# Kernel optimization log

Measured on AMD Instinct MI355X. Metric: run time of the kernel, lower is better.

The kernel has to match this reference:

```python
import jax, jax.numpy as jnp
import numpy as np

E = 1024
H = 16
HD = E // H  # 64


def setup_inputs() -> dict:
    key = jax.random.key(0)
    ks = jax.random.split(key, 5)
    x = jax.random.normal(ks[0], (2, 2048, E), dtype=jnp.float32)
    s = 1.0 / np.sqrt(E)
    W_qkv = jax.random.uniform(ks[1], (E, 3 * E), jnp.float32, -s, s)
    b_qkv = jax.random.uniform(ks[2], (3 * E,), jnp.float32, -s, s)
    W_out = jax.random.uniform(ks[3], (E, E), jnp.float32, -s, s)
    b_out = jax.random.uniform(ks[4], (E,), jnp.float32, -s, s)
    return {"x": x, "W_qkv": W_qkv, "b_qkv": b_qkv, "W_out": W_out, "b_out": b_out}


def reference(x, W_qkv, b_qkv, W_out, b_out):
    B, N, _ = x.shape
    scale = HD ** (-0.5)
    qkv = x @ W_qkv + b_qkv                         # [B, N, 3E]
    qkv = qkv.reshape(B, N, H, 3 * HD)              # torch layout: per-head 3*hd chunk
    qkv = qkv.transpose(0, 2, 1, 3)                 # [B, H, N, 3*hd]
    q, k, v = jnp.split(qkv, 3, axis=-1)            # each [B, H, N, hd]
    attn = jnp.einsum('bhqd,bhkd->bhqk', q, k) * scale
    attn = jax.nn.softmax(attn, axis=-1)            # dropout is identity in eval
    out = jnp.einsum('bhqk,bhkd->bhqd', attn, v)    # [B, H, N, hd]
    out = out.transpose(0, 2, 1, 3).reshape(B, N, E)
    return out @ W_out + b_out
```

## Files before the change

### kernel.cpp

```cpp
#include <hip/hip_runtime.h>


#define SEQ 2048
#define NH  16

typedef __attribute__((ext_vector_type(8))) short short8;
typedef __attribute__((ext_vector_type(4))) short short4v;
typedef __attribute__((ext_vector_type(4))) float floatx4;
typedef __attribute__((ext_vector_type(4))) _Float16 half4;
typedef __attribute__((ext_vector_type(2))) _Float16 half2v;
typedef __attribute__((ext_vector_type(2))) __fp16 fp16x2;

#define QSCALE 0.1803368801111204f

__device__ __forceinline__ short f2bf(float f) {
    union { float f; unsigned u; } v; v.f = f;
    unsigned r = v.u + 0x7fffu + ((v.u >> 16) & 1u);
    return (short)(r >> 16);
}

__device__ __forceinline__ float fast_exp2(float x) {
#if __has_builtin(__builtin_amdgcn_exp2f)
    return __builtin_amdgcn_exp2f(x);
#else
    return exp2f(x);
#endif
}

__device__ __forceinline__ half2v cvt_pk(float a, float b) {
#if __has_builtin(__builtin_amdgcn_cvt_pkrtz)
    union { fp16x2 i; half2v o; } u;
    u.i = __builtin_amdgcn_cvt_pkrtz(a, b);
    return u.o;
#else
    half2v r; r.x = (_Float16)a; r.y = (_Float16)b; return r;
#endif
}

#define GLDS16(gp, lp)                                                          \
    __builtin_amdgcn_global_load_lds(                                           \
        (const __attribute__((address_space(1))) unsigned int*)(gp),            \
        (__attribute__((address_space(3))) unsigned int*)(lp), 16, 0, 0)

__global__ __launch_bounds__(256) void prep_kernel(
    const float* __restrict__ x,  short* __restrict__ xb,
    const float* __restrict__ wq, short* __restrict__ wqkvt,
    const float* __restrict__ wo, short* __restrict__ woutt)
{
    const int tid = threadIdx.x;
    const int b = blockIdx.x;
    if (b < 2048) {
        int i = b * 256 + tid;
        const float4* in4 = (const float4*)x + (size_t)i * 2;
        float4 a = in4[0], c = in4[1];
        short8 o = { f2bf(a.x), f2bf(a.y), f2bf(a.z), f2bf(a.w),
                     f2bf(c.x), f2bf(c.y), f2bf(c.z), f2bf(c.w) };
        *((short8*)xb + i) = o;
        return;
    }
    __shared__ float T[64][65];
    const float* in; short* out; int R, C, c0, r0;
    if (b < 2816) {
        int t = b - 2048; in = wq; out = wqkvt; R = 1024; C = 3072;
        c0 = (t % 48) * 64; r0 = (t / 48) * 64;
    } else {
        int t = b - 2816; in = wo; out = woutt; R = 1024; C = 1024;
        c0 = (t & 15) * 64; r0 = (t >> 4) * 64;
    }
#pragma unroll
    for (int it = 0; it < 4; ++it) {
        int r = it * 16 + (tid >> 4), c = (tid & 15) * 4;
        float4 v = *(const float4*)(in + (size_t)(r0 + r) * C + c0 + c);
        T[c+0][r] = v.x; T[c+1][r] = v.y; T[c+2][r] = v.z; T[c+3][r] = v.w;
    }
    __syncthreads();
#pragma unroll
    for (int it = 0; it < 4; ++it) {
        int oc = it * 16 + (tid >> 4), k = (tid & 15) * 4;
        short4v o = { f2bf(T[oc][k]), f2bf(T[oc][k+1]), f2bf(T[oc][k+2]), f2bf(T[oc][k+3]) };
        *(short4v*)(out + (size_t)(c0 + oc) * R + r0 + k) = o;
    }
}

__global__ __launch_bounds__(256) void vtrans_kernel(
    const _Float16* __restrict__ vn, _Float16* __restrict__ vt)
{
    __shared__ _Float16 T[64][72];
    const int tid = threadIdx.x;
    const int bh = blockIdx.y, n0 = blockIdx.x * 64;
#pragma unroll
    for (int it = 0; it < 2; ++it) {
        int n = it * 32 + (tid >> 3), c = (tid & 7) * 8;
        const _Float16* p = vn + ((size_t)bh * SEQ + n0 + n) * 64 + c;
        half4 a = *(const half4*)(p);
        half4 b = *(const half4*)(p + 4);
        T[c+0][n] = a.x; T[c+1][n] = a.y; T[c+2][n] = a.z; T[c+3][n] = a.w;
        T[c+4][n] = b.x; T[c+5][n] = b.y; T[c+6][n] = b.z; T[c+7][n] = b.w;
    }
    __syncthreads();
#pragma unroll
    for (int it = 0; it < 2; ++it) {
        int idx = it * 256 + tid;
        int quad = idx & 3, d = (idx >> 2) & 63, u = idx >> 8;
        const _Float16* row = &T[d][u * 32 + quad * 4];
        half4 lo = *(const half4*)(row);
        half4 hi = *(const half4*)(row + 16);
        _Float16* q = vt + ((size_t)bh * 64 + d) * SEQ + n0 + u * 32 + quad * 8;
        *(half4*)(q)     = lo;
        *(half4*)(q + 4) = hi;
    }
}

#define GEMM_CORE(A_PTR, B_PTR, LDA, LDB)                                        \
    __shared__ short As[128 * 32];                                               \
    __shared__ short Bs[128 * 32];                                               \
    const int tid  = threadIdx.x;                                                \
    const int lane = tid & 63, w = tid >> 6;                                     \
    const int quad = lane >> 4, l16 = lane & 15;                                 \
    const int wm = w >> 1, wn = w & 1;                                           \
    const int c0 = blockIdx.x * 128, r0 = blockIdx.y * 128;                      \
    floatx4 acc[4][4];                                                           \
    _Pragma("unroll")                                                            \
    for (int i = 0; i < 4; ++i)                                                  \
        _Pragma("unroll")                                                        \
        for (int j = 0; j < 4; ++j) acc[i][j] = (floatx4){0.f, 0.f, 0.f, 0.f};   \
    const int srow = tid >> 2;                                                   \
    const int sgx  = ((tid & 3) ^ ((srow >> 1) & 3)) * 8;                        \
    const short* Ag = (A_PTR) + (size_t)(r0 + srow) * (LDA) + sgx;               \
    const short* Bg = (B_PTR) + (size_t)(c0 + srow) * (LDB) + sgx;               \
    const int fsw = (l16 >> 1) & 3;                                              \
    for (int kk = 0; kk < 1024; kk += 32) {                                      \
        __syncthreads();                                                         \
        GLDS16(Ag + kk,                      As + tid * 8);                      \
        GLDS16(Ag + (size_t)64 * (LDA) + kk, As + 2048 + tid * 8);               \
        GLDS16(Bg + kk,                      Bs + tid * 8);                      \
        GLDS16(Bg + (size_t)64 * (LDB) + kk, Bs + 2048 + tid * 8);               \
        __syncthreads();                                                         \
        short8 af[4], bf[4];                                                     \
        _Pragma("unroll")                                                        \
        for (int mt = 0; mt < 4; ++mt)                                           \
            af[mt] = *(const short8*)&As[(wm * 64 + mt * 16 + l16) * 32 + (quad ^ fsw) * 8]; \
        _Pragma("unroll")                                                        \
        for (int nt = 0; nt < 4; ++nt)                                           \
            bf[nt] = *(const short8*)&Bs[(wn * 64 + nt * 16 + l16) * 32 + (quad ^ fsw) * 8]; \
        _Pragma("unroll")                                                        \
        for (int mt = 0; mt < 4; ++mt)                                           \
            _Pragma("unroll")                                                    \
            for (int nt = 0; nt < 4; ++nt)                                       \
                acc[mt][nt] = __builtin_amdgcn_mfma_f32_16x16x32_bf16(           \
                    af[mt], bf[nt], acc[mt][nt], 0, 0, 0);                       \
    }

__global__ __launch_bounds__(256) void qkv_gemm_kernel(
    const short* __restrict__ wt, const short* __restrict__ xb,
    const float* __restrict__ bias,
    short* __restrict__ qb, short* __restrict__ kb, _Float16* __restrict__ vnb)
{
    GEMM_CORE(wt, xb, 1024, 1024)
#pragma unroll
    for (int mt = 0; mt < 4; ++mt) {
        int oc0 = r0 + wm * 64 + mt * 16 + quad * 4;
        int head = oc0 / 192;
        int t = (oc0 - head * 192) >> 6;
        int d0 = oc0 & 63;
        float4 bv = *(const float4*)(bias + oc0);
#pragma unroll
        for (int nt = 0; nt < 4; ++nt) {
            int tok = c0 + wn * 64 + nt * 16 + l16;
            int bh = (tok >> 11) * NH + head;
            size_t base = ((size_t)bh * SEQ + (tok & (SEQ - 1))) * 64 + d0;
            float v0 = acc[mt][nt][0] + bv.x, v1 = acc[mt][nt][1] + bv.y;
            float v2 = acc[mt][nt][2] + bv.z, v3 = acc[mt][nt][3] + bv.w;
            if (t == 0) {
                short4v o = { f2bf(v0 * QSCALE), f2bf(v1 * QSCALE),
                              f2bf(v2 * QSCALE), f2bf(v3 * QSCALE) };
                *(short4v*)(qb + base) = o;
            } else if (t == 1) {
                short4v o = { f2bf(v0), f2bf(v1), f2bf(v2), f2bf(v3) };
                *(short4v*)(kb + base) = o;
            } else {
                half4 o = { (_Float16)v0, (_Float16)v1, (_Float16)v2, (_Float16)v3 };
                *(half4*)(vnb + base) = o;
            }
        }
    }
}

__global__ __launch_bounds__(512) void out_gemm_kernel(
    const short* __restrict__ wt, const short* __restrict__ ab,
    const float* __restrict__ bias, float* __restrict__ out)
{
    __shared__ short As[128 * 32];
    __shared__ short Bs[128 * 32];
    const int tid  = threadIdx.x;
    const int lane = tid & 63, w = tid >> 6;
    const int quad = lane >> 4, l16 = lane & 15;
    const int wm = w >> 2, wn = w & 3;
    const int c0 = blockIdx.x * 128, r0 = blockIdx.y * 128;
    floatx4 acc[4][2];
#pragma unroll
    for (int i = 0; i < 4; ++i)
#pragma unroll
        for (int j = 0; j < 2; ++j) acc[i][j] = (floatx4){0.f, 0.f, 0.f, 0.f};
    const int srow = tid >> 2;
    const int sgx  = ((tid & 3) ^ ((srow >> 1) & 3)) * 8;
    const short* Ag = wt + (size_t)(r0 + srow) * 1024 + sgx;
    const short* Bg = ab + (size_t)(c0 + srow) * 1024 + sgx;
    const int fsw = (l16 >> 1) & 3;
    for (int kk = 0; kk < 1024; kk += 32) {
        __syncthreads();
        GLDS16(Ag + kk, As + tid * 8);
        GLDS16(Bg + kk, Bs + tid * 8);
        __syncthreads();
        short8 af[4], bf[2];
#pragma unroll
        for (int mt = 0; mt < 4; ++mt)
            af[mt] = *(const short8*)&As[(wm * 64 + mt * 16 + l16) * 32 + (quad ^ fsw) * 8];
#pragma unroll
        for (int nt = 0; nt < 2; ++nt)
            bf[nt] = *(const short8*)&Bs[(wn * 32 + nt * 16 + l16) * 32 + (quad ^ fsw) * 8];
#pragma unroll
        for (int mt = 0; mt < 4; ++mt)
#pragma unroll
            for (int nt = 0; nt < 2; ++nt)
                acc[mt][nt] = __builtin_amdgcn_mfma_f32_16x16x32_bf16(
                    af[mt], bf[nt], acc[mt][nt], 0, 0, 0);
    }
#pragma unroll
    for (int mt = 0; mt < 4; ++mt) {
        int oc0 = r0 + wm * 64 + mt * 16 + quad * 4;
        float4 bv = *(const float4*)(bias + oc0);
#pragma unroll
        for (int nt = 0; nt < 2; ++nt) {
            int tok = c0 + wn * 32 + nt * 16 + l16;
            float4 o = { acc[mt][nt][0] + bv.x, acc[mt][nt][1] + bv.y,
                         acc[mt][nt][2] + bv.z, acc[mt][nt][3] + bv.w };
            *(float4*)(out + (size_t)tok * 1024 + oc0) = o;
        }
    }
}

__global__ __launch_bounds__(256, 4) void attn_kernel(
    const short* __restrict__ qb, const short* __restrict__ kb,
    const _Float16* __restrict__ vtb, short* __restrict__ ob)
{
    __shared__ short    Ks[128 * 64];
    __shared__ _Float16 Vts[64 * 128];
    __shared__ float    Ls[4][32];
    const int tid  = threadIdx.x;
    const int lane = tid & 63, w = tid >> 6;
    const int quad = lane >> 4, l16 = lane & 15;
    const int qh = w >> 1, kq = w & 1;
    const int bh = blockIdx.y;
    const int q0 = blockIdx.x * 64;

    short8 aq[2][2];
#pragma unroll
    for (int qf = 0; qf < 2; ++qf) {
        const short* qp = qb + ((size_t)bh * SEQ + q0 + qh * 32 + qf * 16 + l16) * 64 + quad * 8;
        aq[qf][0] = *(const short8*)(qp);
        aq[qf][1] = *(const short8*)(qp + 32);
    }

    const int krow = tid >> 3, kg = tid & 7;
    const short* kgp = kb + ((size_t)bh * SEQ + krow) * 64 + (kg ^ (krow & 7)) * 8;
    const int vd = tid >> 2, vgg = tid & 3;
    const _Float16* vgp = vtb + ((size_t)bh * 64 + vd) * SEQ + (vgg ^ ((vd >> 1) & 3)) * 8;

    floatx4 o_acc[4][2];
#pragma unroll
    for (int dt = 0; dt < 4; ++dt)
#pragma unroll
        for (int qf = 0; qf < 2; ++qf) o_acc[dt][qf] = (floatx4){0.f, 0.f, 0.f, 0.f};
    float lw[2] = {0.f, 0.f};

    for (int k0 = 0; k0 < SEQ; k0 += 128) {
        __syncthreads();
        const short* kc_p = kgp + (size_t)k0 * 64;
        GLDS16(kc_p,        Ks + tid * 8);
        GLDS16(kc_p + 2048, Ks + 2048 + tid * 8);
        GLDS16(kc_p + 4096, Ks + 4096 + tid * 8);
        GLDS16(kc_p + 6144, Ks + 6144 + tid * 8);
        const _Float16* vc_p = vgp + k0;
        GLDS16((const short*)(vc_p),      (short*)Vts + tid * 8);
        GLDS16((const short*)(vc_p + 32), (short*)Vts + 2048 + tid * 8);
        GLDS16((const short*)(vc_p + 64), (short*)Vts + 4096 + tid * 8);
        GLDS16((const short*)(vc_p + 96), (short*)Vts + 6144 + tid * 8);
        __syncthreads();

#pragma unroll
        for (int uu = 0; uu < 2; ++uu) {
            const int u = kq * 2 + uu;
            half4 avlo[4], avhi[4];
#pragma unroll
            for (int dt = 0; dt < 4; ++dt) {
                union { short8 s; struct { half4 lo; half4 hi; } h; } vv;
                vv.s = *(const short8*)((const short*)Vts + u * 2048
                        + (dt * 16 + l16) * 32 + (quad ^ ((l16 >> 1) & 3)) * 8);
                avlo[dt] = vv.h.lo; avhi[dt] = vv.h.hi;
            }
#pragma unroll
            for (int h = 0; h < 2; ++h) {
                const short* krp = &Ks[(u * 32 + h * 16 + l16) * 64];
                short8 ak0 = *(const short8*)(krp + ((0 + quad) ^ (l16 & 7)) * 8);
                short8 ak1 = *(const short8*)(krp + ((4 + quad) ^ (l16 & 7)) * 8);
                floatx4 sacc[2];
#pragma unroll
                for (int qf = 0; qf < 2; ++qf) {
                    floatx4 z = (floatx4){0.f, 0.f, 0.f, 0.f};
                    z = __builtin_amdgcn_mfma_f32_16x16x32_bf16(ak0, aq[qf][0], z, 0, 0, 0);
                    sacc[qf] = __builtin_amdgcn_mfma_f32_16x16x32_bf16(ak1, aq[qf][1], z, 0, 0, 0);
                }
                half4 pf[2];
#pragma unroll
                for (int qf = 0; qf < 2; ++qf) {
                    float p0 = fast_exp2(sacc[qf][0]);
                    float p1 = fast_exp2(sacc[qf][1]);
                    float p2 = fast_exp2(sacc[qf][2]);
                    float p3 = fast_exp2(sacc[qf][3]);
                    lw[qf] += (p0 + p1) + (p2 + p3);
                    half2v lo = cvt_pk(p0, p1), hi = cvt_pk(p2, p3);
                    pf[qf] = (half4){lo.x, lo.y, hi.x, hi.y};
                }
#pragma unroll
                for (int dt = 0; dt < 4; ++dt)
#pragma unroll
                    for (int qf = 0; qf < 2; ++qf)
                        o_acc[dt][qf] = __builtin_amdgcn_mfma_f32_16x16x16f16(
                            h ? avhi[dt] : avlo[dt], pf[qf], o_acc[dt][qf], 0, 0, 0);
            }
        }
    }

#pragma unroll
    for (int qf = 0; qf < 2; ++qf) {
        lw[qf] += __shfl_xor(lw[qf], 16);
        lw[qf] += __shfl_xor(lw[qf], 32);
        if (quad == 0) Ls[w][qf * 16 + l16] = lw[qf];
    }

    float* Red = (float*)Ks;
    __syncthreads();
#pragma unroll
    for (int dt = 0; dt < 4; ++dt)
#pragma unroll
        for (int qf = 0; qf < 2; ++qf) {
            int fi = (((qh * 2 + qf) * 4 + dt) * 64 + lane) * 4;
            if (kq == 1) *(floatx4*)&Red[fi] = o_acc[dt][qf];
        }
    __syncthreads();
    if (kq == 0) {
        float inv[2];
#pragma unroll
        for (int qf = 0; qf < 2; ++qf) {
            int qi = qf * 16 + l16;
            inv[qf] = 1.0f / (Ls[qh * 2 + 0][qi] + Ls[qh * 2 + 1][qi]);
        }
        const int b = bh >> 4, h = bh & 15;
#pragma unroll
        for (int dt = 0; dt < 4; ++dt)
#pragma unroll
            for (int qf = 0; qf < 2; ++qf) {
                int fi = (((qh * 2 + qf) * 4 + dt) * 64 + lane) * 4;
                floatx4 o = o_acc[dt][qf] + *(const floatx4*)&Red[fi];
                int tok = b * SEQ + q0 + qh * 32 + qf * 16 + l16;
                short4v o4 = { f2bf(o[0] * inv[qf]), f2bf(o[1] * inv[qf]),
                               f2bf(o[2] * inv[qf]), f2bf(o[3] * inv[qf]) };
                *(short4v*)(ob + (size_t)tok * 1024 + h * 64 + dt * 16 + quad * 4) = o4;
            }
    }
}

extern "C" void kernel_launch(void* const* d_in, const int* in_sizes, int n_in,
                              void* d_out, int out_size, void* d_ws, size_t ws_size,
                              hipStream_t stream) {
    const float* x     = (const float*)d_in[0];
    const float* W_qkv = (const float*)d_in[1];
    const float* b_qkv = (const float*)d_in[2];
    const float* W_out = (const float*)d_in[3];
    const float* b_out = (const float*)d_in[4];
    float* out = (float*)d_out;

    short* xb      = (short*)d_ws;
    short* wqkvt   = xb    + (size_t)4096 * 1024;
    short* woutt   = wqkvt + (size_t)3072 * 1024;
    short* qb      = woutt + (size_t)1024 * 1024;
    short* kb      = qb    + (size_t)32 * SEQ * 64;
    _Float16* vnb  = (_Float16*)(kb + (size_t)32 * SEQ * 64);
    _Float16* vtb  = vnb + (size_t)32 * SEQ * 64;
    short* ob      = (short*)(vtb + (size_t)32 * 64 * SEQ);

    prep_kernel<<<3072, 256, 0, stream>>>(x, xb, W_qkv, wqkvt, W_out, woutt);
    qkv_gemm_kernel<<<dim3(32, 24), 256, 0, stream>>>(wqkvt, xb, b_qkv, qb, kb, vnb);
    vtrans_kernel<<<dim3(32, 32), 256, 0, stream>>>(vnb, vtb);
    attn_kernel<<<dim3(32, 32), 256, 0, stream>>>(qb, kb, vtb, ob);
    out_gemm_kernel<<<dim3(32, 8), 512, 0, stream>>>(woutt, ob, b_out, out);
}
```

Baseline: 196.6 us.

## Load V directly from global in attention and share GEMM core for output projection

Result: slower. 265.2 us (+34.9%).

```diff
diff --git a/kernel.cpp b/kernel.cpp
--- a/kernel.cpp
+++ b/kernel.cpp
@@ -186,53 +186,18 @@
     }
 }
 
-__global__ __launch_bounds__(512) void out_gemm_kernel(
+__global__ __launch_bounds__(256) void out_gemm_kernel(
     const short* __restrict__ wt, const short* __restrict__ ab,
     const float* __restrict__ bias, float* __restrict__ out)
 {
-    __shared__ short As[128 * 32];
-    __shared__ short Bs[128 * 32];
-    const int tid  = threadIdx.x;
-    const int lane = tid & 63, w = tid >> 6;
-    const int quad = lane >> 4, l16 = lane & 15;
-    const int wm = w >> 2, wn = w & 3;
-    const int c0 = blockIdx.x * 128, r0 = blockIdx.y * 128;
-    floatx4 acc[4][2];
-#pragma unroll
-    for (int i = 0; i < 4; ++i)
-#pragma unroll
-        for (int j = 0; j < 2; ++j) acc[i][j] = (floatx4){0.f, 0.f, 0.f, 0.f};
-    const int srow = tid >> 2;
-    const int sgx  = ((tid & 3) ^ ((srow >> 1) & 3)) * 8;
-    const short* Ag = wt + (size_t)(r0 + srow) * 1024 + sgx;
-    const short* Bg = ab + (size_t)(c0 + srow) * 1024 + sgx;
-    const int fsw = (l16 >> 1) & 3;
-    for (int kk = 0; kk < 1024; kk += 32) {
-        __syncthreads();
-        GLDS16(Ag + kk, As + tid * 8);
-        GLDS16(Bg + kk, Bs + tid * 8);
-        __syncthreads();
-        short8 af[4], bf[2];
-#pragma unroll
-        for (int mt = 0; mt < 4; ++mt)
-            af[mt] = *(const short8*)&As[(wm * 64 + mt * 16 + l16) * 32 + (quad ^ fsw) * 8];
-#pragma unroll
-        for (int nt = 0; nt < 2; ++nt)
-            bf[nt] = *(const short8*)&Bs[(wn * 32 + nt * 16 + l16) * 32 + (quad ^ fsw) * 8];
-#pragma unroll
-        for (int mt = 0; mt < 4; ++mt)
-#pragma unroll
-            for (int nt = 0; nt < 2; ++nt)
-                acc[mt][nt] = __builtin_amdgcn_mfma_f32_16x16x32_bf16(
-                    af[mt], bf[nt], acc[mt][nt], 0, 0, 0);
-    }
+    GEMM_CORE(wt, ab, 1024, 1024)
 #pragma unroll
     for (int mt = 0; mt < 4; ++mt) {
         int oc0 = r0 + wm * 64 + mt * 16 + quad * 4;
         float4 bv = *(const float4*)(bias + oc0);
 #pragma unroll
-        for (int nt = 0; nt < 2; ++nt) {
-            int tok = c0 + wn * 32 + nt * 16 + l16;
+        for (int nt = 0; nt < 4; ++nt) {
+            int tok = c0 + wn * 64 + nt * 16 + l16;
             float4 o = { acc[mt][nt][0] + bv.x, acc[mt][nt][1] + bv.y,
                          acc[mt][nt][2] + bv.z, acc[mt][nt][3] + bv.w };
             *(float4*)(out + (size_t)tok * 1024 + oc0) = o;
@@ -244,9 +209,8 @@
     const short* __restrict__ qb, const short* __restrict__ kb,
     const _Float16* __restrict__ vtb, short* __restrict__ ob)
 {
-    __shared__ short    Ks[128 * 64];
-    __shared__ _Float16 Vts[64 * 128];
-    __shared__ float    Ls[4][32];
+    __shared__ short Ks[256 * 64];
+    __shared__ float Ls[4][32];
     const int tid  = threadIdx.x;
     const int lane = tid & 63, w = tid >> 6;
     const int quad = lane >> 4, l16 = lane & 15;
@@ -264,8 +228,7 @@
 
     const int krow = tid >> 3, kg = tid & 7;
     const short* kgp = kb + ((size_t)bh * SEQ + krow) * 64 + (kg ^ (krow & 7)) * 8;
-    const int vd = tid >> 2, vgg = tid & 3;
-    const _Float16* vgp = vtb + ((size_t)bh * 64 + vd) * SEQ + (vgg ^ ((vd >> 1) & 3)) * 8;
+    const short* vgp = (const short*)vtb + ((size_t)bh * 64 + l16) * SEQ + quad * 8;
 
     floatx4 o_acc[4][2];
 #pragma unroll
@@ -274,29 +237,22 @@
         for (int qf = 0; qf < 2; ++qf) o_acc[dt][qf] = (floatx4){0.f, 0.f, 0.f, 0.f};
     float lw[2] = {0.f, 0.f};
 
-    for (int k0 = 0; k0 < SEQ; k0 += 128) {
+    for (int k0 = 0; k0 < SEQ; k0 += 256) {
         __syncthreads();
         const short* kc_p = kgp + (size_t)k0 * 64;
-        GLDS16(kc_p,        Ks + tid * 8);
-        GLDS16(kc_p + 2048, Ks + 2048 + tid * 8);
-        GLDS16(kc_p + 4096, Ks + 4096 + tid * 8);
-        GLDS16(kc_p + 6144, Ks + 6144 + tid * 8);
-        const _Float16* vc_p = vgp + k0;
-        GLDS16((const short*)(vc_p),      (short*)Vts + tid * 8);
-        GLDS16((const short*)(vc_p + 32), (short*)Vts + 2048 + tid * 8);
-        GLDS16((const short*)(vc_p + 64), (short*)Vts + 4096 + tid * 8);
-        GLDS16((const short*)(vc_p + 96), (short*)Vts + 6144 + tid * 8);
+#pragma unroll
+        for (int j = 0; j < 8; ++j)
+            GLDS16(kc_p + j * 2048, Ks + j * 2048 + tid * 8);
         __syncthreads();
 
 #pragma unroll
-        for (int uu = 0; uu < 2; ++uu) {
-            const int u = kq * 2 + uu;
+        for (int uu = 0; uu < 4; ++uu) {
+            const int u = kq * 4 + uu;
             half4 avlo[4], avhi[4];
 #pragma unroll
             for (int dt = 0; dt < 4; ++dt) {
                 union { short8 s; struct { half4 lo; half4 hi; } h; } vv;
-                vv.s = *(const short8*)((const short*)Vts + u * 2048
-                        + (dt * 16 + l16) * 32 + (quad ^ ((l16 >> 1) & 3)) * 8);
+                vv.s = *(const short8*)(vgp + (size_t)(dt * 16) * SEQ + k0 + u * 32);
                 avlo[dt] = vv.h.lo; avhi[dt] = vv.h.hi;
             }
 #pragma unroll
@@ -394,5 +350,5 @@
     qkv_gemm_kernel<<<dim3(32, 24), 256, 0, stream>>>(wqkvt, xb, b_qkv, qb, kb, vnb);
     vtrans_kernel<<<dim3(32, 32), 256, 0, stream>>>(vnb, vtb);
     attn_kernel<<<dim3(32, 32), 256, 0, stream>>>(qb, kb, vtb, ob);
-    out_gemm_kernel<<<dim3(32, 8), 512, 0, stream>>>(woutt, ob, b_out, out);
-}
+    out_gemm_kernel<<<dim3(32, 8), 256, 0, stream>>>(woutt, ob, b_out, out);
+}
```
